# Kernel tuning notes

Hardware: AMD Instinct MI355X
Metric: run time of the kernel (lower is better)

Reference implementation:

```python
import jax, jax.numpy as jnp
import numpy as np

D_MODEL = 1024
HEADS = 16
D_FF = 4096
EPS = 1e-6
NEG = -1e9


def setup_inputs() -> dict:
    key = jax.random.key(0)
    ks = jax.random.split(key, 12)
    B, S, D = 2, 2048, D_MODEL
    s = 0.02
    return {
        "x": jax.random.normal(ks[0], (B, S, D), dtype=jnp.float32),
        "mask": jax.random.randint(ks[1], (B, 1, S), 0, 2, dtype=jnp.int32),
        "alpha1": jnp.ones((D,), jnp.float32),
        "bias1": jnp.zeros((D,), jnp.float32),
        "alpha2": jnp.ones((D,), jnp.float32),
        "bias2": jnp.zeros((D,), jnp.float32),
        "Wk": jax.random.normal(ks[2], (D, D), jnp.float32) * s,
        "bk": jnp.zeros((D,), jnp.float32),
        "Wv": jax.random.normal(ks[3], (D, D), jnp.float32) * s,
        "bv": jnp.zeros((D,), jnp.float32),
        "Wo": jax.random.normal(ks[4], (D, D), jnp.float32) * s,
        "bo": jnp.zeros((D,), jnp.float32),
        "W1": jax.random.normal(ks[5], (D, D_FF), jnp.float32) * s,
        "b1": jnp.zeros((D_FF,), jnp.float32),
        "W2": jax.random.normal(ks[6], (D_FF, D), jnp.float32) * s,
        "b2": jnp.zeros((D,), jnp.float32),
    }


def _norm(x, alpha, bias):
    # torch Norm: unbiased std (ddof=1), eps added to std (not variance)
    mu = jnp.mean(x, axis=-1, keepdims=True)
    sd = jnp.std(x, axis=-1, keepdims=True, ddof=1)
    return alpha * (x - mu) / (sd + EPS) + bias


def reference(x, mask, alpha1, bias1, alpha2, bias2,
              Wk, bk, Wv, bv, Wo, bo, W1, b1, W2, b2):
    B, S, D = x.shape
    H, dk = HEADS, D // HEADS

    x2 = _norm(x, alpha1, bias1)
    # NOTE: source bug preserved: q uses k_linear weights
    q = (x2 @ Wk + bk).reshape(B, S, H, dk).transpose(0, 2, 1, 3)  # [B,H,S,dk]
    k = (x2 @ Wk + bk).reshape(B, S, H, dk).transpose(0, 2, 1, 3)
    v = (x2 @ Wv + bv).reshape(B, S, H, dk).transpose(0, 2, 1, 3)

    scores = jnp.einsum('bhqd,bhkd->bhqk', q, k) / jnp.sqrt(jnp.float32(dk))
    scores = jnp.where(mask[:, None, :, :] == 0, NEG, scores)  # [B,1,1,S] broadcast
    attn = jax.nn.softmax(scores, axis=-1)
    ctx = jnp.einsum('bhqk,bhkd->bhqd', attn, v)
    concat = ctx.transpose(0, 2, 1, 3).reshape(B, S, D)
    x = x + (concat @ Wo + bo)

    x2 = _norm(x, alpha2, bias2)
    ff = jax.nn.relu(x2 @ W1 + b1) @ W2 + b2
    return x + ff
```

## Files before the change

kernel.cpp:

```cpp
#include <hip/hip_runtime.h>
#include <hip/hip_bf16.h>
#include <math.h>

typedef __bf16 bf16_t;
typedef __bf16 bf16x8 __attribute__((ext_vector_type(8)));
typedef __bf16 bf16x4 __attribute__((ext_vector_type(4)));
typedef float  f32x4  __attribute__((ext_vector_type(4)));

#define MFMA16(a,b,c) __builtin_amdgcn_mfma_f32_16x16x32_bf16((a),(b),(c),0,0,0)

__device__ static inline void gload_lds16(const void* g, void* l) {
    __builtin_amdgcn_global_load_lds((const __attribute__((address_space(1))) void*)g,
                                     (__attribute__((address_space(3))) void*)l, 16, 0, 0);
}

__device__ static inline float exp2_hw(float x) {
#if __has_builtin(__builtin_amdgcn_exp2f)
    return __builtin_amdgcn_exp2f(x);
#else
    float r; asm("v_exp_f32 %0, %1" : "=v"(r) : "v"(x)); return r;
#endif
}

__device__ static inline float max3f(float a, float b, float c) {
    return fmaxf(fmaxf(a, b), c);
}

__global__ __launch_bounds__(256)
void transpose_f2b(const float* __restrict__ in, bf16_t* __restrict__ out, int R, int C)
{
    __shared__ float t[32][33];
    const int tx = threadIdx.x & 31, ty = threadIdx.x >> 5;
    const int r0 = blockIdx.y << 5, c0 = blockIdx.x << 5;
#pragma unroll
    for (int i = 0; i < 4; ++i)
        t[ty + i*8][tx] = in[(size_t)(r0 + ty + i*8) * C + c0 + tx];
    __syncthreads();
#pragma unroll
    for (int i = 0; i < 4; ++i)
        out[(size_t)(c0 + ty + i*8) * R + r0 + tx] = (bf16_t)t[tx][ty + i*8];
}

__global__ __launch_bounds__(256)
void transpose_b2b(const bf16_t* __restrict__ in, bf16_t* __restrict__ out, int R, int C, int ldi)
{
    __shared__ bf16_t t[32][33];
    const int tx = threadIdx.x & 31, ty = threadIdx.x >> 5;
    const int r0 = blockIdx.y << 5, c0 = blockIdx.x << 5;
#pragma unroll
    for (int i = 0; i < 4; ++i)
        t[ty + i*8][tx] = in[(size_t)(r0 + ty + i*8) * ldi + c0 + tx];
    __syncthreads();
#pragma unroll
    for (int i = 0; i < 4; ++i)
        out[(size_t)(c0 + ty + i*8) * R + r0 + tx] = t[tx][ty + i*8];
}

__global__ __launch_bounds__(256)
void concat_bias(const float* __restrict__ a, const float* __restrict__ b, float* __restrict__ o)
{
    const int i = blockIdx.x * 256 + threadIdx.x;
    o[i] = (i < 1024) ? a[i] : b[i - 1024];
}

__global__ __launch_bounds__(256)
void mask_bias_k(const int* __restrict__ mask, float* __restrict__ mb)
{
    const int i = blockIdx.x * 256 + threadIdx.x;
    mb[i] = (mask[i] == 0) ? -16384.0f : 0.0f;
}

__global__ __launch_bounds__(256)
void layernorm_k(const float* __restrict__ x, const float* __restrict__ gam,
                 const float* __restrict__ bet, bf16_t* __restrict__ out)
{
    const int row = blockIdx.x, tid = threadIdx.x;
    const float4 v = ((const float4*)(x + (size_t)row * 1024))[tid];
    float s  = v.x + v.y + v.z + v.w;
    float ss = v.x*v.x + v.y*v.y + v.z*v.z + v.w*v.w;
#pragma unroll
    for (int off = 32; off >= 1; off >>= 1) {
        s  += __shfl_xor(s,  off);
        ss += __shfl_xor(ss, off);
    }
    __shared__ float rs[4], rq[4];
    if ((tid & 63) == 0) { rs[tid >> 6] = s; rq[tid >> 6] = ss; }
    __syncthreads();
    s  = rs[0] + rs[1] + rs[2] + rs[3];
    ss = rq[0] + rq[1] + rq[2] + rq[3];
    const float mu  = s * (1.0f / 1024.0f);
    const float var = fmaxf((ss - 1024.0f * mu * mu) * (1.0f / 1023.0f), 0.0f);
    const float inv = 1.0f / (sqrtf(var) + 1e-6f);
    const int c = tid << 2;
    bf16x4 o;
    o[0] = (bf16_t)(gam[c+0] * ((v.x - mu) * inv) + bet[c+0]);
    o[1] = (bf16_t)(gam[c+1] * ((v.y - mu) * inv) + bet[c+1]);
    o[2] = (bf16_t)(gam[c+2] * ((v.z - mu) * inv) + bet[c+2]);
    o[3] = (bf16_t)(gam[c+3] * ((v.w - mu) * inv) + bet[c+3]);
    *(bf16x4*)(out + (size_t)row * 1024 + c) = o;
}

template<bool RELU, bool RES, int NFR>
__global__ __launch_bounds__(256, 3)
void gemm128(const bf16_t* __restrict__ A, const bf16_t* __restrict__ Bt,
             const float* __restrict__ bias, const float* __restrict__ res,
             bf16_t* __restrict__ Cb, float* __restrict__ Cf,
             int M, int N, int K)
{
    constexpr int NTILE = NFR * 32;
    __shared__ __align__(16) bf16_t As[128 * 64];
    __shared__ __align__(16) bf16_t Bs[NTILE * 64];
    const int tid  = threadIdx.x;
    const int lane = tid & 63;
    const int wid  = tid >> 6;
    const int wr = wid >> 1, wc = wid & 1;
    const int ntn = N / NTILE;
    const int cpx = gridDim.x >> 3;
    const int swz = (blockIdx.x & 7) * cpx + (blockIdx.x >> 3);
    const int bm = (swz / ntn) << 7;
    const int bn = (swz % ntn) * NTILE;
    const int l15 = lane & 15;
    const int g   = lane >> 4;

    f32x4 acc[4][NFR];
#pragma unroll
    for (int i = 0; i < 4; ++i)
#pragma unroll
        for (int j = 0; j < NFR; ++j)
#pragma unroll
            for (int e = 0; e < 4; ++e) acc[i][j][e] = 0.0f;

    const int srow = tid >> 3;
    const int scb  = (((tid & 7) << 4) ^ ((srow & 7) << 4));
    const bf16_t* Ab = A  + (size_t)(bm + srow) * K + (scb >> 1);
    const bf16_t* Bb = Bt + (size_t)(bn + srow) * K + (scb >> 1);
    bf16_t* AsB = As + wid * 512;
    bf16_t* BsB = Bs + wid * 512;

    const int nK = K >> 6;
    for (int kt = 0; kt < nK; ++kt) {
        const int k0 = kt << 6;
#pragma unroll
        for (int it = 0; it < 4; ++it)
            gload_lds16(Ab + k0 + (size_t)(it * 32) * K, AsB + it * 2048);
#pragma unroll
        for (int it = 0; it < NFR; ++it)
            gload_lds16(Bb + k0 + (size_t)(it * 32) * K, BsB + it * 2048);
        __syncthreads();

        bf16x8 af[4][2], bfr[NFR][2];
#pragma unroll
        for (int mi = 0; mi < 4; ++mi) {
            const int ar = (wr << 6) + mi * 16 + l15;
#pragma unroll
            for (int ks = 0; ks < 2; ++ks) {
                const int kb = (ks << 6) + (g << 4);
                af[mi][ks] = *(const bf16x8*)((const char*)As + ar * 128 + (kb ^ ((ar & 7) << 4)));
            }
        }
#pragma unroll
        for (int ni = 0; ni < NFR; ++ni) {
            const int br = wc * (NFR * 16) + ni * 16 + l15;
#pragma unroll
            for (int ks = 0; ks < 2; ++ks) {
                const int kb = (ks << 6) + (g << 4);
                bfr[ni][ks] = *(const bf16x8*)((const char*)Bs + br * 128 + (kb ^ ((br & 7) << 4)));
            }
        }
#pragma unroll
        for (int mi = 0; mi < 4; ++mi)
#pragma unroll
            for (int ni = 0; ni < NFR; ++ni) {
                acc[mi][ni] = MFMA16(af[mi][0], bfr[ni][0], acc[mi][ni]);
                acc[mi][ni] = MFMA16(af[mi][1], bfr[ni][1], acc[mi][ni]);
            }
        __syncthreads();
    }

#pragma unroll
    for (int mi = 0; mi < 4; ++mi)
#pragma unroll
        for (int ni = 0; ni < NFR; ++ni) {
            const int gc = bn + wc * (NFR * 16) + ni * 16 + l15;
            const float bv = bias[gc];
#pragma unroll
            for (int j = 0; j < 4; ++j) {
                const int gr = bm + (wr << 6) + mi * 16 + (g << 2) + j;
                float vv = acc[mi][ni][j] + bv;
                if (RELU) vv = fmaxf(vv, 0.0f);
                if (RES)  Cf[(size_t)gr * N + gc] = vv + res[(size_t)gr * N + gc];
                else      Cb[(size_t)gr * N + gc] = (bf16_t)vv;
            }
        }
}

__global__ __launch_bounds__(256, 3)
void attn_kernel(const bf16_t* __restrict__ qkv, const bf16_t* __restrict__ vT,
                 const float* __restrict__ mbias, bf16_t* __restrict__ ctx)
{
    __shared__ __align__(16) bf16_t Ks[2][64 * 64];
    __shared__ __align__(16) bf16_t Vs[2][64 * 64];
    __shared__ __align__(16) char   Ps[4][4096];

    const int tid = threadIdx.x, lane = tid & 63, wid = tid >> 6;
    const int l15 = lane & 15, g = lane >> 4;
    const int id = blockIdx.x;
    const int qt = (id >> 3) & 15;
    const int bh = (id & 7) * 4 + (id >> 7);
    const int b = bh >> 4, h = bh & 15;
    const size_t rowQ = (size_t)(b * 2048 + qt * 128 + wid * 32);
    const float C = 0.18033688f;

    bf16x8 qf[2][2];
#pragma unroll
    for (int qfi = 0; qfi < 2; ++qfi)
#pragma unroll
        for (int ks = 0; ks < 2; ++ks)
            qf[qfi][ks] = *(const bf16x8*)(qkv + (rowQ + qfi*16 + l15) * 2048
                                           + h*64 + ks*32 + g*8);

    bf16x8 vones;
#pragma unroll
    for (int e = 0; e < 8; ++e) vones[e] = (bf16_t)1.0f;

    f32x4 O[2][4], l_acc[2];
#pragma unroll
    for (int mf = 0; mf < 2; ++mf) {
#pragma unroll
        for (int df = 0; df < 4; ++df)
#pragma unroll
            for (int e = 0; e < 4; ++e) O[mf][df][e] = 0.0f;
#pragma unroll
        for (int e = 0; e < 4; ++e) l_acc[mf][e] = 0.0f;
    }
    float m_t[2] = {0.0f, 0.0f};

    const int srow = tid >> 3;
    const int scb  = (((tid & 7) << 4) ^ ((srow & 7) << 4));
    const bf16_t* Kb = qkv + (size_t)(b*2048 + srow) * 2048 + h*64 + (scb >> 1);
    const bf16_t* Vb = vT  + (size_t)(h*64 + srow) * 4096 + b*2048 + (scb >> 1);
    const float*  Mb = mbias + b*2048;
    bf16_t* Ks0 = Ks[0] + wid * 512;  bf16_t* Ks1 = Ks[1] + wid * 512;
    bf16_t* Vs0 = Vs[0] + wid * 512;  bf16_t* Vs1 = Vs[1] + wid * 512;

    #define STAGE(KD, VD, KT)                                        \
        do {                                                         \
            gload_lds16(Kb + (size_t)(KT) * 2048, (KD));             \
            gload_lds16(Kb + (size_t)((KT) + 32) * 2048, (KD) + 2048);\
            gload_lds16(Vb + (KT), (VD));                            \
            gload_lds16(Vb + (size_t)32 * 4096 + (KT), (VD) + 2048); \
        } while (0)

    STAGE(Ks0, Vs0, 0);
    __syncthreads();

    char* Pw = Ps[wid];

    for (int kt_i = 0; kt_i < 32; ++kt_i) {
        const int kt = kt_i << 6;
        const bool cur1 = (kt_i & 1);
        if (kt_i < 31) {
            if (cur1) STAGE(Ks0, Vs0, kt + 64);
            else      STAGE(Ks1, Vs1, kt + 64);
        }
        const char* Kc = (const char*)(cur1 ? Ks[1] : Ks[0]);
        const char* Vc = (const char*)(cur1 ? Vs[1] : Vs[0]);

        bf16x8 kf[4][2];
#pragma unroll
        for (int kfi = 0; kfi < 4; ++kfi) {
            const int kr = kfi*16 + l15;
#pragma unroll
            for (int ks = 0; ks < 2; ++ks)
                kf[kfi][ks] = *(const bf16x8*)(Kc + kr*128
                                               + ((ks*64 + g*16) ^ ((kr & 7) << 4)));
        }
        f32x4 st[4][2];
#pragma unroll
        for (int kfi = 0; kfi < 4; ++kfi)
#pragma unroll
            for (int qfi = 0; qfi < 2; ++qfi) {
                f32x4 t;
#pragma unroll
                for (int e = 0; e < 4; ++e) t[e] = 0.0f;
                t = MFMA16(kf[kfi][0], qf[qfi][0], t);
                t = MFMA16(kf[kfi][1], qf[qfi][1], t);
                st[kfi][qfi] = t;
            }

        bf16x8 vf[4][2];
#pragma unroll
        for (int df = 0; df < 4; ++df) {
            const int vr = df*16 + l15;
#pragma unroll
            for (int ks = 0; ks < 2; ++ks)
                vf[df][ks] = *(const bf16x8*)(Vc + vr*128
                                              + ((ks*64 + g*16) ^ ((vr & 7) << 4)));
        }

#pragma unroll
        for (int kfi = 0; kfi < 4; ++kfi) {
            const float4 bb = *(const float4*)(Mb + kt + kfi*16 + g*4);
            const float* bj = (const float*)&bb;
#pragma unroll
            for (int j = 0; j < 4; ++j)
#pragma unroll
                for (int qfi = 0; qfi < 2; ++qfi)
                    st[kfi][qfi][j] = fmaf(st[kfi][qfi][j], C, bj[j]);
        }
        float mx[2];
#pragma unroll
        for (int qfi = 0; qfi < 2; ++qfi) {
            const float t0 = max3f(st[0][qfi][0], st[0][qfi][1], st[0][qfi][2]);
            const float t1 = max3f(st[0][qfi][3], st[1][qfi][0], st[1][qfi][1]);
            const float t2 = max3f(st[1][qfi][2], st[1][qfi][3], st[2][qfi][0]);
            const float t3 = max3f(st[2][qfi][1], st[2][qfi][2], st[2][qfi][3]);
            const float t4 = max3f(st[3][qfi][0], st[3][qfi][1], st[3][qfi][2]);
            float mxq = fmaxf(max3f(t0, t1, t2), max3f(t3, t4, st[3][qfi][3]));
            mxq = fmaxf(mxq, __shfl_xor(mxq, 16));
            mxq = fmaxf(mxq, __shfl_xor(mxq, 32));
            mx[qfi] = mxq;
        }
        if (__any((mx[0] > m_t[0] + 8.0f) || (mx[1] > m_t[1] + 8.0f))) {
            float cr[2];
#pragma unroll
            for (int qfi = 0; qfi < 2; ++qfi) {
                const float mn = fmaxf(m_t[qfi], mx[qfi]);
                cr[qfi] = exp2_hw(m_t[qfi] - mn);
                m_t[qfi] = mn;
            }
#pragma unroll
            for (int mf = 0; mf < 2; ++mf)
#pragma unroll
                for (int j = 0; j < 4; ++j) {
                    const float cj = __shfl(cr[mf], g*4 + j);
#pragma unroll
                    for (int df = 0; df < 4; ++df) O[mf][df][j] *= cj;
                    l_acc[mf][j] *= cj;
                }
        }
#pragma unroll
        for (int qfi = 0; qfi < 2; ++qfi) {
            const int q = qfi*16 + l15;
#pragma unroll
            for (int kfi = 0; kfi < 4; ++kfi) {
                bf16x4 pk;
#pragma unroll
                for (int j = 0; j < 4; ++j)
                    pk[j] = (bf16_t)exp2_hw(st[kfi][qfi][j] - m_t[qfi]);
                *(bf16x4*)(Pw + q*128 + ((kfi*32 + g*8) ^ ((l15 & 7) << 4))) = pk;
            }
        }
        bf16x8 pa[2][2];
#pragma unroll
        for (int mf = 0; mf < 2; ++mf) {
            const int r = mf*16 + l15;
#pragma unroll
            for (int ks = 0; ks < 2; ++ks)
                pa[mf][ks] = *(const bf16x8*)(Pw + r*128 + ((ks*64 + g*16) ^ ((l15 & 7) << 4)));
        }
#pragma unroll
        for (int mf = 0; mf < 2; ++mf) {
#pragma unroll
            for (int df = 0; df < 4; ++df) {
                O[mf][df] = MFMA16(pa[mf][0], vf[df][0], O[mf][df]);
                O[mf][df] = MFMA16(pa[mf][1], vf[df][1], O[mf][df]);
            }
            l_acc[mf] = MFMA16(pa[mf][0], vones, l_acc[mf]);
            l_acc[mf] = MFMA16(pa[mf][1], vones, l_acc[mf]);
        }
        __syncthreads();
    }
    #undef STAGE

#pragma unroll
    for (int mf = 0; mf < 2; ++mf)
#pragma unroll
        for (int j = 0; j < 4; ++j) {
            const float ri = __builtin_amdgcn_rcpf(l_acc[mf][j]);
            const size_t gr = rowQ + mf*16 + g*4 + j;
#pragma unroll
            for (int df = 0; df < 4; ++df)
                ctx[gr * 1024 + h*64 + df*16 + l15] = (bf16_t)(O[mf][df][j] * ri);
        }
}

extern "C" void kernel_launch(void* const* d_in, const int* in_sizes, int n_in,
                              void* d_out, int out_size, void* d_ws, size_t ws_size,
                              hipStream_t stream)
{
    const float* x   = (const float*)d_in[0];
    const int*   msk = (const int*)  d_in[1];
    const float* a1  = (const float*)d_in[2];
    const float* be1 = (const float*)d_in[3];
    const float* a2  = (const float*)d_in[4];
    const float* be2 = (const float*)d_in[5];
    const float* Wk  = (const float*)d_in[6];
    const float* bk  = (const float*)d_in[7];
    const float* Wv  = (const float*)d_in[8];
    const float* bv  = (const float*)d_in[9];
    const float* Wo  = (const float*)d_in[10];
    const float* bo  = (const float*)d_in[11];
    const float* W1  = (const float*)d_in[12];
    const float* b1  = (const float*)d_in[13];
    const float* W2  = (const float*)d_in[14];
    const float* b2  = (const float*)d_in[15];
    float* out = (float*)d_out;

    char* ws = (char*)d_ws;
    const size_t MB = 1u << 20;
    if (ws_size < 78 * MB) return;
    bf16_t* WkT = (bf16_t*)(ws + 0 * MB);
    bf16_t* WvT = (bf16_t*)(ws + 2 * MB);
    bf16_t* WoT = (bf16_t*)(ws + 4 * MB);
    bf16_t* W1T = (bf16_t*)(ws + 6 * MB);
    bf16_t* W2T = (bf16_t*)(ws + 14 * MB);
    bf16_t* x2  = (bf16_t*)(ws + 22 * MB);
    bf16_t* qkv = (bf16_t*)(ws + 30 * MB);
    bf16_t* vTb = (bf16_t*)(ws + 46 * MB);
    bf16_t* ctx = (bf16_t*)(ws + 54 * MB);
    float*  xn  = (float*) (ws + 62 * MB);
    float*  bkv   = (float*)(ws + 62 * MB);
    float*  mbias = (float*)(ws + 62 * MB + 32768);
    bf16_t* hb  = (bf16_t*)(ws + 30 * MB);

    dim3 blk(256);
    transpose_f2b<<<dim3(32, 32),  blk, 0, stream>>>(Wk, WkT, 1024, 1024);
    transpose_f2b<<<dim3(32, 32),  blk, 0, stream>>>(Wv, WvT, 1024, 1024);
    transpose_f2b<<<dim3(32, 32),  blk, 0, stream>>>(Wo, WoT, 1024, 1024);
    transpose_f2b<<<dim3(128, 32), blk, 0, stream>>>(W1, W1T, 1024, 4096);
    transpose_f2b<<<dim3(32, 128), blk, 0, stream>>>(W2, W2T, 4096, 1024);
    concat_bias<<<8, blk, 0, stream>>>(bk, bv, bkv);
    mask_bias_k<<<16, blk, 0, stream>>>(msk, mbias);

    layernorm_k<<<4096, blk, 0, stream>>>(x, a1, be1, x2);
    gemm128<false,false,4><<<dim3(32 * 16), blk, 0, stream>>>(x2, WkT, bkv, nullptr, qkv, nullptr, 4096, 2048, 1024);
    transpose_b2b<<<dim3(32, 128), blk, 0, stream>>>(qkv + 1024, vTb, 4096, 1024, 2048);
    attn_kernel<<<dim3(512), blk, 0, stream>>>(qkv, vTb, mbias, ctx);
    gemm128<false,true,2><<<dim3(32 * 16), blk, 0, stream>>>(ctx, WoT, bo, x,  nullptr, xn, 4096, 1024, 1024);
    layernorm_k<<<4096, blk, 0, stream>>>(xn, a2, be2, x2);
    gemm128<true,false,4><<<dim3(32 * 32), blk, 0, stream>>>(x2, W1T, b1, nullptr, hb, nullptr, 4096, 4096, 1024);
    gemm128<false,true,2><<<dim3(32 * 16), blk, 0, stream>>>(hb, W2T, b2, xn, nullptr, out, 4096, 1024, 4096);
}
```

Before: 245.5 us.

## Double-buffer LDS tiles in GEMM to overlap global loads with MFMA

Adds a double-buffered mode to the bf16 GEMM. The next K-tile is staged into the alternate LDS buffer while the current one is computed, which removes one barrier per iteration and hides load latency. It is enabled for the QKV, Wo and W2 GEMMs, while the W1 GEMM keeps single buffering. The launch-bounds occupancy hint drops from 3 to 2 blocks per SIMD to make room for the extra LDS and registers, which can lower latency hiding through occupancy.

```diff
diff --git a/kernel.cpp b/kernel.cpp
--- a/kernel.cpp
+++ b/kernel.cpp
@@ -100,16 +100,17 @@
     *(bf16x4*)(out + (size_t)row * 1024 + c) = o;
 }
 
-template<bool RELU, bool RES, int NFR>
-__global__ __launch_bounds__(256, 3)
+template<bool RELU, bool RES, int NFR, bool DBUF>
+__global__ __launch_bounds__(256, 2)
 void gemm128(const bf16_t* __restrict__ A, const bf16_t* __restrict__ Bt,
              const float* __restrict__ bias, const float* __restrict__ res,
              bf16_t* __restrict__ Cb, float* __restrict__ Cf,
              int M, int N, int K)
 {
     constexpr int NTILE = NFR * 32;
-    __shared__ __align__(16) bf16_t As[128 * 64];
-    __shared__ __align__(16) bf16_t Bs[NTILE * 64];
+    constexpr int NBUF = DBUF ? 2 : 1;
+    __shared__ __align__(16) bf16_t As[NBUF][128 * 64];
+    __shared__ __align__(16) bf16_t Bs[NBUF][NTILE * 64];
     const int tid  = threadIdx.x;
     const int lane = tid & 63;
     const int wid  = tid >> 6;
@@ -134,20 +135,20 @@
     const int scb  = (((tid & 7) << 4) ^ ((srow & 7) << 4));
     const bf16_t* Ab = A  + (size_t)(bm + srow) * K + (scb >> 1);
     const bf16_t* Bb = Bt + (size_t)(bn + srow) * K + (scb >> 1);
-    bf16_t* AsB = As + wid * 512;
-    bf16_t* BsB = Bs + wid * 512;
-
-    const int nK = K >> 6;
-    for (int kt = 0; kt < nK; ++kt) {
+
+    auto stage = [&](int buf, int kt) {
         const int k0 = kt << 6;
+        bf16_t* AsB = As[buf] + wid * 512;
+        bf16_t* BsB = Bs[buf] + wid * 512;
 #pragma unroll
         for (int it = 0; it < 4; ++it)
             gload_lds16(Ab + k0 + (size_t)(it * 32) * K, AsB + it * 2048);
 #pragma unroll
         for (int it = 0; it < NFR; ++it)
             gload_lds16(Bb + k0 + (size_t)(it * 32) * K, BsB + it * 2048);
-        __syncthreads();
-
+    };
+
+    auto compute = [&](int buf) {
         bf16x8 af[4][2], bfr[NFR][2];
 #pragma unroll
         for (int mi = 0; mi < 4; ++mi) {
@@ -155,7 +156,7 @@
 #pragma unroll
             for (int ks = 0; ks < 2; ++ks) {
                 const int kb = (ks << 6) + (g << 4);
-                af[mi][ks] = *(const bf16x8*)((const char*)As + ar * 128 + (kb ^ ((ar & 7) << 4)));
+                af[mi][ks] = *(const bf16x8*)((const char*)As[buf] + ar * 128 + (kb ^ ((ar & 7) << 4)));
             }
         }
 #pragma unroll
@@ -164,7 +165,7 @@
 #pragma unroll
             for (int ks = 0; ks < 2; ++ks) {
                 const int kb = (ks << 6) + (g << 4);
-                bfr[ni][ks] = *(const bf16x8*)((const char*)Bs + br * 128 + (kb ^ ((br & 7) << 4)));
+                bfr[ni][ks] = *(const bf16x8*)((const char*)Bs[buf] + br * 128 + (kb ^ ((br & 7) << 4)));
             }
         }
 #pragma unroll
@@ -174,7 +175,25 @@
                 acc[mi][ni] = MFMA16(af[mi][0], bfr[ni][0], acc[mi][ni]);
                 acc[mi][ni] = MFMA16(af[mi][1], bfr[ni][1], acc[mi][ni]);
             }
+    };
+
+    const int nK = K >> 6;
+    if constexpr (DBUF) {
+        stage(0, 0);
         __syncthreads();
+        for (int kt = 0; kt < nK; ++kt) {
+            const int cur = kt & 1;
+            if (kt + 1 < nK) stage(cur ^ 1, kt + 1);
+            compute(cur);
+            __syncthreads();
+        }
+    } else {
+        for (int kt = 0; kt < nK; ++kt) {
+            stage(0, kt);
+            __syncthreads();
+            compute(0);
+            __syncthreads();
+        }
     }
 
 #pragma unroll
@@ -434,11 +453,11 @@
     mask_bias_k<<<16, blk, 0, stream>>>(msk, mbias);
 
     layernorm_k<<<4096, blk, 0, stream>>>(x, a1, be1, x2);
-    gemm128<false,false,4><<<dim3(32 * 16), blk, 0, stream>>>(x2, WkT, bkv, nullptr, qkv, nullptr, 4096, 2048, 1024);
+    gemm128<false,false,4,true><<<dim3(32 * 16), blk, 0, stream>>>(x2, WkT, bkv, nullptr, qkv, nullptr, 4096, 2048, 1024);
     transpose_b2b<<<dim3(32, 128), blk, 0, stream>>>(qkv + 1024, vTb, 4096, 1024, 2048);
     attn_kernel<<<dim3(512), blk, 0, stream>>>(qkv, vTb, mbias, ctx);
-    gemm128<false,true,2><<<dim3(32 * 16), blk, 0, stream>>>(ctx, WoT, bo, x,  nullptr, xn, 4096, 1024, 1024);
+    gemm128<false,true,2,true><<<dim3(32 * 16), blk, 0, stream>>>(ctx, WoT, bo, x,  nullptr, xn, 4096, 1024, 1024);
     layernorm_k<<<4096, blk, 0, stream>>>(xn, a2, be2, x2);
-    gemm128<true,false,4><<<dim3(32 * 32), blk, 0, stream>>>(x2, W1T, b1, nullptr, hb, nullptr, 4096, 4096, 1024);
-    gemm128<false,true,2><<<dim3(32 * 16), blk, 0, stream>>>(hb, W2T, b2, xn, nullptr, out, 4096, 1024, 4096);
-}
+    gemm128<true,false,4,false><<<dim3(32 * 32), blk, 0, stream>>>(x2, W1T, b1, nullptr, hb, nullptr, 4096, 4096, 1024);
+    gemm128<false,true,2,true><<<dim3(32 * 16), blk, 0, stream>>>(hb, W2T, b2, xn, nullptr, out, 4096, 1024, 4096);
+}
```

Measured after the change: 242.2 us. Within noise of the previous version (-1.3%).
